# Optimization experiments

Measured on AMD Instinct MI355X. Metric: run time of the kernel, lower is better.

Reference implementation:

```python
import jax, jax.numpy as jnp
import numpy as np

TIM_SIZE, TIM_EMB = 48, 64
APP_SIZE, APP_EMB = 10000, 256
UID_SIZE, UID_EMB = 10000, 256
INPUT_SIZE = TIM_EMB + APP_EMB  # 320
S = 4096
N = S - 3  # windows of length 4


def setup_inputs() -> dict:
    key = jax.random.key(0)
    ks = jax.random.split(key, 12)
    inp = {
        "tim": jax.random.randint(ks[0], (S, 1), 0, TIM_SIZE),
        "app": jax.random.uniform(ks[1], (S, APP_SIZE), dtype=jnp.float32),
        "loc": jax.random.randint(ks[2], (S, 1), 0, 1),
        "uid": jax.random.randint(ks[3], (1,), 0, UID_SIZE),
        "ptim": jax.random.randint(ks[4], (N, 1), 0, TIM_SIZE),
        # learned parameters
        "emb_tim_w": jax.random.normal(ks[5], (TIM_SIZE, TIM_EMB), dtype=jnp.float32) * 0.02,
        "emb_uid_w": jax.random.normal(ks[6], (UID_SIZE, UID_EMB), dtype=jnp.float32) * 0.02,
        "emb_app_w": jax.random.normal(ks[7], (APP_SIZE, APP_EMB), dtype=jnp.float32) * 0.02,
        "attn_W": jax.random.uniform(ks[8], (INPUT_SIZE, 1), dtype=jnp.float32),
        "attn_b": jax.random.uniform(ks[9], (4, 1), dtype=jnp.float32),
        "attn_fc_w": jax.random.normal(ks[10], (APP_EMB, INPUT_SIZE), dtype=jnp.float32) * 0.02,
        "attn_fc_b": jnp.zeros((APP_EMB,), dtype=jnp.float32),
        "dec_w": jax.random.normal(ks[11], (APP_SIZE, APP_EMB + TIM_EMB), dtype=jnp.float32) * 0.02,
        "dec_b": jnp.zeros((APP_SIZE,), dtype=jnp.float32),
    }
    return inp


def reference(tim, app, loc, uid, ptim, emb_tim_w, emb_uid_w, emb_app_w,
              attn_W, attn_b, attn_fc_w, attn_fc_b, dec_w, dec_b):
    # embeddings (squeeze(1) in torch)
    tim_emb = emb_tim_w[tim[:, 0]]    # [S, TIM_EMB]
    ptim_emb = emb_tim_w[ptim[:, 0]]  # [N, TIM_EMB]
    # 'sum' app embedding mode: multi-hot @ table
    app_emb = app @ emb_app_w         # [S, APP_EMB]
    x = jnp.concatenate([app_emb, tim_emb], axis=1)  # [S, INPUT_SIZE]; dropout is identity at eval
    # sliding windows of length 4 (vectorizes the torch per-i loop)
    n = tim.shape[0] - 3
    idx = jnp.arange(n)[:, None] + jnp.arange(4)[None, :]  # [N, 4]
    win = x[idx]                                          # [N, 4, INPUT_SIZE]
    H = jnp.tanh(win @ attn_W + attn_b)                   # [N, 4, 1]
    Xn = H / jnp.sum(jnp.abs(H), axis=(1, 2), keepdims=True)  # L1 normalize over the window
    pooled = jnp.einsum('nf,nfd->nd', Xn[:, :, 0], win)   # [N, INPUT_SIZE]
    out = pooled @ attn_fc_w.T + attn_fc_b                # [N, APP_EMB]
    uid_emb = emb_uid_w[uid[0]]                           # [APP_EMB], broadcast = repeat
    out = out * uid_emb
    out = jnp.concatenate([out, ptim_emb], axis=1)        # [N, APP_EMB+TIM_EMB]
    score = jax.nn.sigmoid(out @ dec_w.T + dec_b)         # [N, APP_SIZE]
    return score
```

## Files before the change

kernel.cpp:

```cpp
#include <hip/hip_runtime.h>

typedef __attribute__((ext_vector_type(8))) short  bf16x8;
typedef __attribute__((ext_vector_type(8))) unsigned short u16x8;
typedef __attribute__((ext_vector_type(4))) float  f32x4;

constexpr int S    = 4096;
constexpr int NR   = 4093;
constexpr int KAPP = 10000;
constexpr int EAPP = 256;
constexpr int ETIM = 64;
constexpr int DIN  = 320;
constexpr int NDEC = 10000;
constexpr int NSK  = 8;
constexpr int KCH  = 1248;
constexpr int NS   = 39;
constexpr int TAILK= 9984;
constexpr int KPAD = 10240;

__device__ inline unsigned short f2bf(float f) {
    unsigned u = __float_as_uint(f);
    u += 0x7fffu + ((u >> 16) & 1u);
    return (unsigned short)(u >> 16);
}
__device__ inline float bf2f(unsigned short h) {
    return __uint_as_float(((unsigned)h) << 16);
}
__device__ inline u16x8 pack8(f32x4 a, f32x4 b) {
    u16x8 v;
    v[0]=f2bf(a.x); v[1]=f2bf(a.y); v[2]=f2bf(a.z); v[3]=f2bf(a.w);
    v[4]=f2bf(b.x); v[5]=f2bf(b.y); v[6]=f2bf(b.z); v[7]=f2bf(b.w);
    return v;
}
__device__ inline bf16x8 as_bf(u16x8 v) {
    union { u16x8 u; bf16x8 b; } c; c.u = v; return c.b;
}

__global__ __launch_bounds__(256) void k_cvt_bf16(
    const float* __restrict__ in, unsigned short* __restrict__ out, int n8)
{
    int id = blockIdx.x * 256 + threadIdx.x;
    if (id >= n8) return;
    const float* p = in + (size_t)id * 8;
    f32x4 a = *reinterpret_cast<const f32x4*>(p);
    f32x4 b = *reinterpret_cast<const f32x4*>(p + 4);
    *reinterpret_cast<u16x8*>(out + (size_t)id * 8) = pack8(a, b);
}

__global__ __launch_bounds__(256) void k_bake_appw(
    const float* __restrict__ B, unsigned short* __restrict__ Bpp)
{
    __shared__ float T[64][68];
    const int kt = blockIdx.x * 64, nt = blockIdx.y * 64;
    const int tid = threadIdx.x;
    #pragma unroll
    for (int i = 0; i < 4; ++i) {
        int c = tid + (i << 8);
        int k = c >> 4, n4 = (c & 15) << 2;
        f32x4 v = {0.f, 0.f, 0.f, 0.f};
        if (kt + k < KAPP)
            v = *reinterpret_cast<const f32x4*>(&B[(size_t)(kt + k) * EAPP + nt + n4]);
        *reinterpret_cast<f32x4*>(&T[k][n4]) = v;
    }
    __syncthreads();
    #pragma unroll
    for (int i = 0; i < 2; ++i) {
        int c = tid + (i << 8);
        int ln = c & 63, lc = c >> 6;
        int t = (kt >> 5) + (lc >> 2), ck = lc & 3;
        u16x8 v;
        #pragma unroll
        for (int h = 0; h < 8; ++h) v[h] = f2bf(T[(lc << 3) + h][ln]);
        *reinterpret_cast<u16x8*>(
            &Bpp[((size_t)t * 1024 + (ck << 8) + nt + ln) * 8]) = v;
    }
}

__global__ __launch_bounds__(256) void k_embed_tim(
    const int* __restrict__ tim, const float* __restrict__ emb_tim,
    unsigned short* __restrict__ xb)
{
    int r = blockIdx.x * 4 + (threadIdx.x >> 6);
    int e = threadIdx.x & 63;
    xb[(size_t)r * DIN + EAPP + e] = f2bf(emb_tim[tim[r] * ETIM + e]);
}
__global__ __launch_bounds__(256) void k_embed_ptim(
    const int* __restrict__ ptim, const float* __restrict__ emb_tim,
    unsigned short* __restrict__ yb)
{
    int r = blockIdx.x * 4 + (threadIdx.x >> 6);
    int e = threadIdx.x & 63;
    if (r < NR) yb[(size_t)r * DIN + EAPP + e] = f2bf(emb_tim[ptim[r] * ETIM + e]);
}

__global__ __launch_bounds__(256, 2) void k_app(
    const float* __restrict__ A, const unsigned short* __restrict__ Bpp,
    float* __restrict__ part)
{
    __shared__ float          Afs[3][1024];
    __shared__ unsigned short Bs[3][8192];
    const int tid = threadIdx.x, lane = tid & 63, w = tid >> 6;
    const int ks = blockIdx.x, bm = blockIdx.y << 5;
    const int wc = w << 6, rl = lane & 15, kq = lane >> 4;
    const int k0 = ks * KCH;

    const int ap = (w << 6) + lane;
    const float* gA = A + (size_t)(bm + (ap & 31)) * KAPP + k0 + ((ap >> 5) << 2);
    const unsigned short* gB = Bpp + ((size_t)(ks * NS) << 13) + (lane << 3);

#define STAGE(T, BUF) do {                                                      \
    __builtin_amdgcn_global_load_lds(                                           \
        (const __attribute__((address_space(1))) void*)(gA + ((T) << 5)),       \
        (__attribute__((address_space(3))) void*)(&Afs[BUF][w << 8]),           \
        16, 0, 0);                                                              \
    const unsigned short* sB_ = gB + ((size_t)(T) << 13);                       \
    _Pragma("unroll")                                                           \
    for (int q = 0; q < 4; ++q)                                                 \
        __builtin_amdgcn_global_load_lds(                                       \
            (const __attribute__((address_space(1))) void*)(sB_ +               \
                ((((w << 2) + q)) << 9)),                                       \
            (__attribute__((address_space(3))) void*)(                          \
                &Bs[BUF][(((w << 2) + q)) << 9]),                               \
            16, 0, 0);                                                          \
} while (0)

#define COMPUTE(BUF) do {                                                       \
    bf16x8 af_[2], bf_[4];                                                      \
    _Pragma("unroll")                                                           \
    for (int i = 0; i < 2; ++i) {                                               \
        f32x4 lo_ = *reinterpret_cast<const f32x4*>(                            \
            &Afs[BUF][(((kq << 1)    ) * 32 + (i << 4) + rl) << 2]);            \
        f32x4 hi_ = *reinterpret_cast<const f32x4*>(                            \
            &Afs[BUF][(((kq << 1) + 1) * 32 + (i << 4) + rl) << 2]);            \
        af_[i] = as_bf(pack8(lo_, hi_));                                        \
    }                                                                           \
    _Pragma("unroll")                                                           \
    for (int j = 0; j < 4; ++j)                                                 \
        bf_[j] = *reinterpret_cast<const bf16x8*>(                              \
            &Bs[BUF][((kq << 8) + wc + (j << 4) + rl) << 3]);                   \
    _Pragma("unroll")                                                           \
    for (int i = 0; i < 2; ++i)                                                 \
        _Pragma("unroll")                                                       \
        for (int j = 0; j < 4; ++j)                                             \
            acc[i][j] = __builtin_amdgcn_mfma_f32_16x16x32_bf16(                \
                af_[i], bf_[j], acc[i][j], 0, 0, 0);                            \
} while (0)

    f32x4 acc[2][4];
    #pragma unroll
    for (int i = 0; i < 2; ++i)
        #pragma unroll
        for (int j = 0; j < 4; ++j) acc[i][j] = (f32x4){0.f, 0.f, 0.f, 0.f};

    STAGE(0, 0);
    STAGE(1, 1);
    int b0 = 0;
    for (int t = 0; t < NS - 2; ++t) {
        int b2 = b0 + 2; if (b2 >= 3) b2 -= 3;
        asm volatile("s_waitcnt vmcnt(5)" ::: "memory");
        __builtin_amdgcn_s_barrier();
        __builtin_amdgcn_sched_barrier(0);
        STAGE(t + 2, b2);
        __builtin_amdgcn_sched_barrier(0);
        COMPUTE(b0);
        ++b0; if (b0 == 3) b0 = 0;
    }
    asm volatile("s_waitcnt vmcnt(5)" ::: "memory");
    __builtin_amdgcn_s_barrier();
    COMPUTE(b0);
    ++b0; if (b0 == 3) b0 = 0;
    asm volatile("s_waitcnt vmcnt(0)" ::: "memory");
    __builtin_amdgcn_s_barrier();
    COMPUTE(b0);
#undef STAGE
#undef COMPUTE

    float* P = part + ((size_t)ks * S + bm) * EAPP;
    const int rq = kq << 2;
    #pragma unroll
    for (int i = 0; i < 2; ++i)
        #pragma unroll
        for (int j = 0; j < 4; ++j) {
            int col = wc + j * 16 + rl;
            #pragma unroll
            for (int q = 0; q < 4; ++q)
                __builtin_nontemporal_store(acc[i][j][q],
                    &P[(size_t)(i * 16 + rq + q) * EAPP + col]);
        }
}

__global__ __launch_bounds__(256) void k_reduce_app(
    const float* __restrict__ part, const float* __restrict__ A,
    const unsigned short* __restrict__ Bpp, unsigned short* __restrict__ xb)
{
    int id = blockIdx.x * 256 + threadIdx.x;
    int row = id >> 6, c4 = (id & 63) << 2;
    f32x4 s = {0.f, 0.f, 0.f, 0.f};
    #pragma unroll
    for (int sl = 0; sl < NSK; ++sl) {
        f32x4 v = __builtin_nontemporal_load(reinterpret_cast<const f32x4*>(
            &part[((size_t)sl * S + row) * EAPP + c4]));
        s.x += v.x; s.y += v.y; s.z += v.z; s.w += v.w;
    }
    #pragma unroll
    for (int ck = 0; ck < 2; ++ck) {
        f32x4 a0 = *reinterpret_cast<const f32x4*>(&A[(size_t)row * KAPP + TAILK + (ck << 3)]);
        f32x4 a1 = *reinterpret_cast<const f32x4*>(&A[(size_t)row * KAPP + TAILK + (ck << 3) + 4]);
        float av[8] = {a0.x, a0.y, a0.z, a0.w, a1.x, a1.y, a1.z, a1.w};
        #pragma unroll
        for (int e = 0; e < 4; ++e) {
            u16x8 bv = *reinterpret_cast<const u16x8*>(
                &Bpp[((size_t)(312 * 1024 + (ck << 8) + c4 + e)) * 8]);
            float t = 0.f;
            #pragma unroll
            for (int h = 0; h < 8; ++h) t = fmaf(av[h], bf2f(bv[h]), t);
            s[e] += t;
        }
    }
    unsigned short* o = &xb[(size_t)row * DIN + c4];
    o[0] = f2bf(s.x); o[1] = f2bf(s.y); o[2] = f2bf(s.z); o[3] = f2bf(s.w);
}

__global__ __launch_bounds__(256) void k_score(
    const unsigned short* __restrict__ xb, const float* __restrict__ W,
    float* __restrict__ s)
{
    int wv = threadIdx.x >> 6, lane = threadIdx.x & 63;
    int m = blockIdx.x * 4 + wv;
    float sum = 0.f;
    #pragma unroll
    for (int i = 0; i < 5; ++i) {
        int k = lane + (i << 6);
        sum += bf2f(xb[(size_t)m * DIN + k]) * W[k];
    }
    #pragma unroll
    for (int off = 32; off; off >>= 1) sum += __shfl_down(sum, off);
    if (lane == 0) s[m] = sum;
}

__global__ void k_pooled(
    const unsigned short* __restrict__ xb, const float* __restrict__ s,
    const float* __restrict__ attn_b, unsigned short* __restrict__ pooledb)
{
    int n = blockIdx.x, d = threadIdx.x;
    float h[4], den = 0.f;
    #pragma unroll
    for (int f = 0; f < 4; ++f) {
        h[f] = tanhf(s[n + f] + attn_b[f]);
        den += fabsf(h[f]);
    }
    float inv = 1.f / den, p = 0.f;
    #pragma unroll
    for (int f = 0; f < 4; ++f)
        p = fmaf(h[f] * inv, bf2f(xb[(size_t)(n + f) * DIN + d]), p);
    pooledb[(size_t)n * DIN + d] = f2bf(p);
}

template<int EPI>
__global__ __launch_bounds__(256, 4) void k_nt320(
    const unsigned short* __restrict__ A, const unsigned short* __restrict__ B,
    int Nb, int Mlim,
    const float* __restrict__ bias,
    const float* __restrict__ emb_uid, const int* __restrict__ uid,
    void* __restrict__ Cout, int ldc)
{
    __shared__ unsigned short As[40 * 64 * 8];
    const int tid = threadIdx.x, lane = tid & 63, w = tid >> 6;
    const int qx = gridDim.x >> 3;
    const int swz = (blockIdx.x & 7) * qx + (blockIdx.x >> 3);
    const int nbn = (Nb + 255) >> 8;
    const int bm = (swz / nbn) << 6, bn = (swz % nbn) << 8;
    const int rl = lane & 15, kq = lane >> 4;
    const int wc = w << 6;

    {
        const int row = tid >> 2, c0 = tid & 3;
        const unsigned short* src = A + (size_t)(bm + row) * DIN;
        #pragma unroll
        for (int t = 0; t < 10; ++t) {
            int ck = c0 + (t << 2);
            *reinterpret_cast<u16x8*>(&As[((ck << 6) + row) << 3]) =
                *reinterpret_cast<const u16x8*>(src + (ck << 3));
        }
    }
    __syncthreads();

    f32x4 acc[4][4];
    #pragma unroll
    for (int i = 0; i < 4; ++i)
        #pragma unroll
        for (int j = 0; j < 4; ++j) acc[i][j] = (f32x4){0.f, 0.f, 0.f, 0.f};

    u16x8 b0[4], b1[4];
#define LOADB(DST, KSN) do {                                                    \
    const int kg_ = ((KSN) << 5) + (kq << 3);                                   \
    _Pragma("unroll")                                                           \
    for (int j = 0; j < 4; ++j) {                                               \
        int brow = bn + wc + j * 16 + rl;                                       \
        u16x8 v_ = {0,0,0,0,0,0,0,0};                                           \
        if (brow < Nb)                                                          \
            v_ = *reinterpret_cast<const u16x8*>(&B[(size_t)brow * DIN + kg_]); \
        DST[j] = v_;                                                            \
    }                                                                           \
} while (0)

#define STEPNT(BARR, KSN) do {                                                  \
    const int ckb_ = (((KSN) << 2) + kq) << 6;                                  \
    bf16x8 af_[4];                                                              \
    _Pragma("unroll")                                                           \
    for (int i = 0; i < 4; ++i)                                                 \
        af_[i] = *reinterpret_cast<const bf16x8*>(                              \
            &As[(ckb_ + i * 16 + rl) << 3]);                                    \
    _Pragma("unroll")                                                           \
    for (int i = 0; i < 4; ++i)                                                 \
        _Pragma("unroll")                                                       \
        for (int j = 0; j < 4; ++j)                                             \
            acc[i][j] = __builtin_amdgcn_mfma_f32_16x16x32_bf16(                \
                af_[i], as_bf(BARR[j]), acc[i][j], 0, 0, 0);                     \
} while (0)

    LOADB(b0, 0);
    LOADB(b1, 1);
    #pragma unroll
    for (int p = 0; p < 5; ++p) {
        STEPNT(b0, 2 * p);
        if (2 * p + 2 < 10) LOADB(b0, 2 * p + 2);
        STEPNT(b1, 2 * p + 1);
        if (2 * p + 3 < 10) LOADB(b1, 2 * p + 3);
    }
#undef LOADB
#undef STEPNT

    const int rq = kq << 2;
    if (EPI == 1) {
        unsigned short* C = (unsigned short*)Cout;
        const float* us = emb_uid + (size_t)uid[0] * EAPP;
        #pragma unroll
        for (int j = 0; j < 4; ++j) {
            int col = bn + wc + j * 16 + rl;
            if (col >= Nb) continue;
            float um = us[col], bb = bias[col];
            #pragma unroll
            for (int i = 0; i < 4; ++i)
                #pragma unroll
                for (int q = 0; q < 4; ++q) {
                    int row = bm + i * 16 + rq + q;
                    if (row < Mlim)
                        C[(size_t)row * ldc + col] = f2bf((acc[i][j][q] + bb) * um);
                }
        }
    } else {
        float* C = (float*)Cout;
        float* epi = reinterpret_cast<float*>(As);
        float bb[4];
        #pragma unroll
        for (int j = 0; j < 4; ++j) {
            int col = bn + wc + j * 16 + rl;
            bb[j] = (col < Nb) ? bias[col] : 0.f;
        }
        const int r16 = tid >> 6, c4 = (tid & 63) << 2;
        #pragma unroll
        for (int i = 0; i < 4; ++i) {
            __syncthreads();
            #pragma unroll
            for (int j = 0; j < 4; ++j) {
                int colL = wc + j * 16 + rl;
                #pragma unroll
                for (int q = 0; q < 4; ++q) {
                    float v = acc[i][j][q] + bb[j];
                    epi[(rq + q) * 260 + colL] = 1.f / (1.f + __expf(-v));
                }
            }
            __syncthreads();
            #pragma unroll
            for (int r4 = 0; r4 < 4; ++r4) {
                int rowL = (r4 << 2) + r16;
                int grow = bm + (i << 4) + rowL;
                f32x4 v = *reinterpret_cast<const f32x4*>(&epi[rowL * 260 + c4]);
                if (grow < Mlim) {
                    if (bn + 256 <= Nb) {
                        __builtin_nontemporal_store(v,
                            reinterpret_cast<f32x4*>(&C[(size_t)grow * ldc + bn + c4]));
                    } else {
                        #pragma unroll
                        for (int e = 0; e < 4; ++e)
                            if (bn + c4 + e < Nb)
                                __builtin_nontemporal_store(v[e],
                                    &C[(size_t)grow * ldc + bn + c4 + e]);
                    }
                }
            }
        }
    }
}

extern "C" void kernel_launch(void* const* d_in, const int* in_sizes, int n_in,
                              void* d_out, int out_size, void* d_ws, size_t ws_size,
                              hipStream_t stream)
{
    const int*   tim       = (const int*)  d_in[0];
    const float* app       = (const float*)d_in[1];
    const int*   uid       = (const int*)  d_in[3];
    const int*   ptim      = (const int*)  d_in[4];
    const float* emb_tim_w = (const float*)d_in[5];
    const float* emb_uid_w = (const float*)d_in[6];
    const float* emb_app_w = (const float*)d_in[7];
    const float* attn_W    = (const float*)d_in[8];
    const float* attn_b    = (const float*)d_in[9];
    const float* attn_fc_w = (const float*)d_in[10];
    const float* attn_fc_b = (const float*)d_in[11];
    const float* dec_w     = (const float*)d_in[12];
    const float* dec_b     = (const float*)d_in[13];
    float* out = (float*)d_out;

    char* w = (char*)d_ws;
    size_t o = 0;
    auto alloc = [&](size_t bytes) { char* p = w + o; o = (o + bytes + 511) & ~(size_t)511; return p; };
    unsigned short* xb      = (unsigned short*)alloc((size_t)S * DIN * 2);
    unsigned short* pooledb = (unsigned short*)alloc((size_t)S * DIN * 2);
    unsigned short* yb      = (unsigned short*)alloc((size_t)S * DIN * 2);
    float*          s       = (float*)        alloc((size_t)S * 4);
    unsigned short* Bpp     = (unsigned short*)alloc((size_t)EAPP * KPAD * 2);
    unsigned short* decb    = (unsigned short*)alloc((size_t)NDEC * DIN * 2);
    unsigned short* fcb     = (unsigned short*)alloc((size_t)EAPP * DIN * 2);
    float*          part    = (float*)        alloc((size_t)NSK * S * EAPP * 4);

    k_cvt_bf16<<<(NDEC * DIN / 8 + 255) / 256, 256, 0, stream>>>(dec_w, decb, NDEC * DIN / 8);
    k_cvt_bf16<<<(EAPP * DIN / 8 + 255) / 256, 256, 0, stream>>>(attn_fc_w, fcb, EAPP * DIN / 8);
    dim3 gT(KPAD / 64, EAPP / 64);
    k_bake_appw<<<gT, 256, 0, stream>>>(emb_app_w, Bpp);
    k_embed_tim<<<S / 4, 256, 0, stream>>>(tim, emb_tim_w, xb);

    dim3 gApp(NSK, S / 32);
    k_app<<<gApp, 256, 0, stream>>>(app, Bpp, part);
    k_reduce_app<<<S * 64 / 256, 256, 0, stream>>>(part, app, Bpp, xb);

    k_score<<<S / 4, 256, 0, stream>>>(xb, attn_W, s);
    k_pooled<<<NR, DIN, 0, stream>>>(xb, s, attn_b, pooledb);
    k_embed_ptim<<<S / 4, 256, 0, stream>>>(ptim, emb_tim_w, yb);

    k_nt320<1><<<64, 256, 0, stream>>>(pooledb, fcb, EAPP, S,
                                       attn_fc_b, emb_uid_w, uid, yb, DIN);
    k_nt320<2><<<40 * 64, 256, 0, stream>>>(yb, decb, NDEC, NR,
                                            dec_b, nullptr, nullptr, out, NDEC);
}
```

Baseline: 221.4 us.

## Load A operand directly to registers with triple-buffered prefetch in k_app

The fp32 A operand of the app-embedding GEMM no longer goes through LDS. Each lane loads its own fragment straight into registers, using three rotating register sets with one-step prefetch, while B stays staged in LDS with direct global-to-LDS loads. The main loop is unrolled by three so register sets and LDS buffers rotate statically. Removing the A shared buffer lowers LDS use, which allows raising the launch-bounds occupancy hint from 2 to 3 blocks, at the cost of more registers held by in-flight A prefetches and less coalesced A global accesses.

```diff
diff --git a/kernel.cpp b/kernel.cpp
--- a/kernel.cpp
+++ b/kernel.cpp
@@ -92,26 +92,26 @@
     if (r < NR) yb[(size_t)r * DIN + EAPP + e] = f2bf(emb_tim[ptim[r] * ETIM + e]);
 }
 
-__global__ __launch_bounds__(256, 2) void k_app(
+__global__ __launch_bounds__(256, 3) void k_app(
     const float* __restrict__ A, const unsigned short* __restrict__ Bpp,
     float* __restrict__ part)
 {
-    __shared__ float          Afs[3][1024];
     __shared__ unsigned short Bs[3][8192];
     const int tid = threadIdx.x, lane = tid & 63, w = tid >> 6;
     const int ks = blockIdx.x, bm = blockIdx.y << 5;
     const int wc = w << 6, rl = lane & 15, kq = lane >> 4;
-    const int k0 = ks * KCH;
-
-    const int ap = (w << 6) + lane;
-    const float* gA = A + (size_t)(bm + (ap & 31)) * KAPP + k0 + ((ap >> 5) << 2);
+    const int kO = ks * KCH;
     const unsigned short* gB = Bpp + ((size_t)(ks * NS) << 13) + (lane << 3);
 
-#define STAGE(T, BUF) do {                                                      \
-    __builtin_amdgcn_global_load_lds(                                           \
-        (const __attribute__((address_space(1))) void*)(gA + ((T) << 5)),       \
-        (__attribute__((address_space(3))) void*)(&Afs[BUF][w << 8]),           \
-        16, 0, 0);                                                              \
+    f32x4 acc[2][4];
+    #pragma unroll
+    for (int i = 0; i < 2; ++i)
+        #pragma unroll
+        for (int j = 0; j < 4; ++j) acc[i][j] = (f32x4){0.f, 0.f, 0.f, 0.f};
+
+    f32x4 a0[2][2], a1[2][2], a2[2][2];
+
+#define STAGEB(T, BUF) do {                                                     \
     const unsigned short* sB_ = gB + ((size_t)(T) << 13);                       \
     _Pragma("unroll")                                                           \
     for (int q = 0; q < 4; ++q)                                                 \
@@ -123,16 +123,21 @@
             16, 0, 0);                                                          \
 } while (0)
 
-#define COMPUTE(BUF) do {                                                       \
+#define LOADA(T, SET) do {                                                      \
+    _Pragma("unroll")                                                           \
+    for (int i = 0; i < 2; ++i) {                                               \
+        const float* p_ = A + (size_t)(bm + (i << 4) + rl) * KAPP               \
+                            + kO + ((T) << 5) + (kq << 3);                      \
+        SET[i][0] = *reinterpret_cast<const f32x4*>(p_);                        \
+        SET[i][1] = *reinterpret_cast<const f32x4*>(p_ + 4);                    \
+    }                                                                           \
+} while (0)
+
+#define COMPUTE(SET, BUF) do {                                                  \
     bf16x8 af_[2], bf_[4];                                                      \
     _Pragma("unroll")                                                           \
-    for (int i = 0; i < 2; ++i) {                                               \
-        f32x4 lo_ = *reinterpret_cast<const f32x4*>(                            \
-            &Afs[BUF][(((kq << 1)    ) * 32 + (i << 4) + rl) << 2]);            \
-        f32x4 hi_ = *reinterpret_cast<const f32x4*>(                            \
-            &Afs[BUF][(((kq << 1) + 1) * 32 + (i << 4) + rl) << 2]);            \
-        af_[i] = as_bf(pack8(lo_, hi_));                                        \
-    }                                                                           \
+    for (int i = 0; i < 2; ++i)                                                 \
+        af_[i] = as_bf(pack8(SET[i][0], SET[i][1]));                            \
     _Pragma("unroll")                                                           \
     for (int j = 0; j < 4; ++j)                                                 \
         bf_[j] = *reinterpret_cast<const bf16x8*>(                              \
@@ -145,34 +150,38 @@
                 af_[i], bf_[j], acc[i][j], 0, 0, 0);                            \
 } while (0)
 
-    f32x4 acc[2][4];
-    #pragma unroll
-    for (int i = 0; i < 2; ++i)
-        #pragma unroll
-        for (int j = 0; j < 4; ++j) acc[i][j] = (f32x4){0.f, 0.f, 0.f, 0.f};
-
-    STAGE(0, 0);
-    STAGE(1, 1);
-    int b0 = 0;
-    for (int t = 0; t < NS - 2; ++t) {
-        int b2 = b0 + 2; if (b2 >= 3) b2 -= 3;
-        asm volatile("s_waitcnt vmcnt(5)" ::: "memory");
-        __builtin_amdgcn_s_barrier();
-        __builtin_amdgcn_sched_barrier(0);
-        STAGE(t + 2, b2);
-        __builtin_amdgcn_sched_barrier(0);
-        COMPUTE(b0);
-        ++b0; if (b0 == 3) b0 = 0;
-    }
-    asm volatile("s_waitcnt vmcnt(5)" ::: "memory");
+#define PH(T, ACUR, ANXT, BUF, BUF2) do {                                       \
+    asm volatile("s_waitcnt vmcnt(8)" ::: "memory");                            \
+    __builtin_amdgcn_s_barrier();                                               \
+    __builtin_amdgcn_sched_barrier(0);                                          \
+    LOADA((T) + 1, ANXT);                                                       \
+    STAGEB((T) + 2, BUF2);                                                      \
+    __builtin_amdgcn_sched_barrier(0);                                          \
+    COMPUTE(ACUR, BUF);                                                         \
+} while (0)
+
+    STAGEB(0, 0);
+    LOADA(0, a0);
+    STAGEB(1, 1);
+    for (int it = 0; it < 12; ++it) {
+        PH(it * 3 + 0, a0, a1, 0, 2);
+        PH(it * 3 + 1, a1, a2, 1, 0);
+        PH(it * 3 + 2, a2, a0, 2, 1);
+    }
+    PH(36, a0, a1, 0, 2);
+    asm volatile("s_waitcnt vmcnt(8)" ::: "memory");
     __builtin_amdgcn_s_barrier();
-    COMPUTE(b0);
-    ++b0; if (b0 == 3) b0 = 0;
-    asm volatile("s_waitcnt vmcnt(0)" ::: "memory");
+    __builtin_amdgcn_sched_barrier(0);
+    LOADA(38, a2);
+    __builtin_amdgcn_sched_barrier(0);
+    COMPUTE(a1, 1);
+    asm volatile("s_waitcnt vmcnt(4)" ::: "memory");
     __builtin_amdgcn_s_barrier();
-    COMPUTE(b0);
-#undef STAGE
+    COMPUTE(a2, 2);
+#undef STAGEB
+#undef LOADA
 #undef COMPUTE
+#undef PH
 
     float* P = part + ((size_t)ks * S + bm) * EAPP;
     const int rq = kq << 2;
```

Result: slower. 248.7 us (+12.3%).
